# Optimization experiments

Hardware: AMD Instinct MI355X
Metric: run time of the kernel (lower is better)

The kernel has to match this reference:

```python
import jax, jax.numpy as jnp
import numpy as np

D_MODEL = 2048
N_HEADS = 32
N_KV_HEADS = 8
D_K = D_MODEL // N_HEADS
HEADS_PER_GROUP = N_HEADS // N_KV_HEADS
B, S = 2, 2048


def setup_inputs() -> dict:
    key = jax.random.key(0)
    ks = jax.random.split(key, 12)
    scale = 1.0 / np.sqrt(D_MODEL)
    inp = {
        "q": jax.random.normal(ks[0], (B, S, D_MODEL), jnp.float32),
        "k": jax.random.normal(ks[1], (B, S, D_MODEL), jnp.float32),
        "v": jax.random.normal(ks[2], (B, S, D_MODEL), jnp.float32),
        # causal mask, broadcastable over [B, H, S, S]
        "mask": jnp.tril(jnp.ones((S, S), jnp.bool_))[None, None],
        # torch Linear convention: W [out, in], y = x @ W.T + b
        "Wq": jax.random.normal(ks[3], (D_MODEL, D_MODEL), jnp.float32) * scale,
        "bq": jax.random.normal(ks[4], (D_MODEL,), jnp.float32) * 0.01,
        "Wk": jax.random.normal(ks[5], (N_KV_HEADS * D_K, D_MODEL), jnp.float32) * scale,
        "bk": jax.random.normal(ks[6], (N_KV_HEADS * D_K,), jnp.float32) * 0.01,
        "Wv": jax.random.normal(ks[7], (N_KV_HEADS * D_K, D_MODEL), jnp.float32) * scale,
        "bv": jax.random.normal(ks[8], (N_KV_HEADS * D_K,), jnp.float32) * 0.01,
        "Wo": jax.random.normal(ks[9], (D_MODEL, D_MODEL), jnp.float32) * scale,
        "bo": jax.random.normal(ks[10], (D_MODEL,), jnp.float32) * 0.01,
    }
    return inp


def reference(q, k, v, mask, Wq, bq, Wk, bk, Wv, bv, Wo, bo):
    b, s, _ = q.shape
    # projections (torch Linear: x @ W.T + b)
    query = q @ Wq.T + bq                      # [B, S, D]
    key = k @ Wk.T + bk                        # [B, S, Kv*dk]
    value = v @ Wv.T + bv
    # [B, Kv, G, S, dk] for query (group heads per kv head instead of repeating K/V)
    query = query.reshape(b, s, N_KV_HEADS, HEADS_PER_GROUP, D_K).transpose(0, 2, 3, 1, 4)
    key = key.reshape(b, s, N_KV_HEADS, D_K).transpose(0, 2, 1, 3)      # [B, Kv, S, dk]
    value = value.reshape(b, s, N_KV_HEADS, D_K).transpose(0, 2, 1, 3)  # [B, Kv, S, dk]
    scores = jnp.einsum('bkgqd,bksd->bkgqs', query, key) / jnp.sqrt(jnp.float32(D_K))
    # mask is [1,1,S,S] broadcastable; add group axis
    scores = jnp.where(mask[:, :, None], scores, jnp.float32(-1e9))
    attn = jax.nn.softmax(scores, axis=-1)     # dropout p=0.0 -> identity
    out = jnp.einsum('bkgqs,bksd->bkgqd', attn, value)  # [B, Kv, G, S, dk]
    out = out.transpose(0, 3, 1, 2, 4).reshape(b, s, D_MODEL)
    return out @ Wo.T + bo
```

## Files before the change

### kernel.cpp

```cpp
#include <hip/hip_runtime.h>
#include <cstdint>

#define D_MODEL 2048
#define NKV 8
#define GQ 4
#define DK 64
#define B_ 2
#define S_ 2048
#define MS (B_*S_)
#define KVD (NKV*DK)

typedef unsigned short u16;
typedef __attribute__((ext_vector_type(8))) short bf16x8;
typedef __attribute__((ext_vector_type(4))) short bf16x4;
typedef __attribute__((ext_vector_type(4))) float f32x4;
typedef __attribute__((ext_vector_type(16))) float f32x16;
typedef __attribute__((ext_vector_type(4))) unsigned short u16x4;

__device__ __forceinline__ u16 f2bf(float f) {
    union { float f; uint32_t u; } x; x.f = f;
    uint32_t u = x.u;
    uint32_t r = (u + 0x7FFFu + ((u >> 16) & 1u)) >> 16;
    return (u16)r;
}
__device__ __forceinline__ float bf2f(u16 h) {
    union { uint32_t u; float f; } x; x.u = ((uint32_t)h) << 16;
    return x.f;
}

__device__ __forceinline__ void gload_lds16(const void* g, void* lds) {
    __builtin_amdgcn_global_load_lds(
        (const __attribute__((address_space(1))) void*)g,
        (__attribute__((address_space(3))) void*)lds, 16, 0, 0);
}

__device__ __forceinline__ bf16x8 cvt8(float4 a, float4 b) {
    union { unsigned u[4]; bf16x8 v; } r;
    asm("v_cvt_pk_bf16_f32 %0, %1, %2" : "=v"(r.u[0]) : "v"(a.x), "v"(a.y));
    asm("v_cvt_pk_bf16_f32 %0, %1, %2" : "=v"(r.u[1]) : "v"(a.z), "v"(a.w));
    asm("v_cvt_pk_bf16_f32 %0, %1, %2" : "=v"(r.u[2]) : "v"(b.x), "v"(b.y));
    asm("v_cvt_pk_bf16_f32 %0, %1, %2" : "=v"(r.u[3]) : "v"(b.z), "v"(b.w));
    return r.v;
}

__global__ __launch_bounds__(256, 3)
void gemm_qkv(const float* __restrict__ Aq, const float* __restrict__ Ak,
              const float* __restrict__ Av,
              const float* __restrict__ Wq, const float* __restrict__ Wk,
              const float* __restrict__ Wv,
              const float* __restrict__ bq, const float* __restrict__ bk,
              const float* __restrict__ bv,
              u16* __restrict__ Qp, u16* __restrict__ Kp, u16* __restrict__ Vt) {
    __shared__ __align__(16) u16 SA[2][128 * 32];
    __shared__ __align__(16) u16 SB[2][128 * 32];
    const int tid = threadIdx.x;
    const int lane = tid & 63;
    const int fr = lane & 15, fq = lane >> 4;
    const int w = tid >> 6;
    const int wr = w >> 1, wc = w & 1;
    const int K = D_MODEL, NT = K / 32;

    const int bid = blockIdx.x;
    const int sw = (bid & 7) * 96 + (bid >> 3);
    const float* A; const float* Bw; const float* bias;
    int seg, by, bx;
    if (sw < 512)      { seg = 0; A = Aq; Bw = Wq; bias = bq; by = sw >> 4;         bx = sw & 15; }
    else if (sw < 640) { seg = 1; A = Ak; Bw = Wk; bias = bk; by = (sw - 512) >> 2; bx = (sw - 512) & 3; }
    else               { seg = 2; A = Av; Bw = Wv; bias = bv; by = (sw - 640) >> 2; bx = (sw - 640) & 3; }
    const int m0 = by * 128, n0 = bx * 128;

    const int sr = tid >> 2, sc = tid & 3;
    float4 ra[2][2], rb[2][2];
    auto LOADA = [&](int t) {
        const float* p0 = A + (size_t)(m0 + sr) * K + (t << 5) + sc * 8;
#pragma unroll
        for (int j = 0; j < 2; ++j) {
            const float* p = p0 + (size_t)(j * 64) * K;
            ra[j][0] = *(const float4*)p; ra[j][1] = *(const float4*)(p + 4);
        }
    };
    auto LOADB = [&](int t) {
        const float* p0 = Bw + (size_t)(n0 + sr) * K + (t << 5) + sc * 8;
#pragma unroll
        for (int j = 0; j < 2; ++j) {
            const float* p = p0 + (size_t)(j * 64) * K;
            rb[j][0] = *(const float4*)p; rb[j][1] = *(const float4*)(p + 4);
        }
    };
    auto WRITE = [&](int q) {
#pragma unroll
        for (int j = 0; j < 2; ++j) {
            int row = j * 64 + sr;
            int s = (sc ^ ((row >> 1) & 3)) << 4;
            *(bf16x8*)((char*)&SA[q][0] + row * 64 + s) = cvt8(ra[j][0], ra[j][1]);
            *(bf16x8*)((char*)&SB[q][0] + row * 64 + s) = cvt8(rb[j][0], rb[j][1]);
        }
    };

    f32x4 acc[4][4] = {};
    const int arow = wr * 64, brow = wc * 64;

    LOADA(0); LOADB(0);
    WRITE(0);
    LOADA(1); LOADB(1);
    asm volatile("s_waitcnt lgkmcnt(0)" ::: "memory");
    __builtin_amdgcn_s_barrier();

    for (int t = 0; t < NT; ++t) {
        const int q = t & 1;
        if (t + 1 < NT) WRITE(q ^ 1);
        if (t + 2 < NT) { LOADA(t + 2); LOADB(t + 2); }
        const char* sa = (const char*)&SA[q][0];
        const char* sb = (const char*)&SB[q][0];
        bf16x8 af[4], bfr[4];
#pragma unroll
        for (int m = 0; m < 4; ++m) {
            int row = arow + m * 16 + fr;
            af[m] = *(const bf16x8*)(sa + row * 64 + ((fq ^ ((row >> 1) & 3)) << 4));
        }
#pragma unroll
        for (int n = 0; n < 4; ++n) {
            int row = brow + n * 16 + fr;
            bfr[n] = *(const bf16x8*)(sb + row * 64 + ((fq ^ ((row >> 1) & 3)) << 4));
        }
        __builtin_amdgcn_s_setprio(1);
#pragma unroll
        for (int m = 0; m < 4; ++m)
#pragma unroll
            for (int n = 0; n < 4; ++n)
                acc[m][n] = __builtin_amdgcn_mfma_f32_16x16x32_bf16(af[m], bfr[n], acc[m][n], 0, 0, 0);
        __builtin_amdgcn_s_setprio(0);
        asm volatile("s_waitcnt lgkmcnt(0)" ::: "memory");
        __builtin_amdgcn_s_barrier();
    }

    float bvv[4];
#pragma unroll
    for (int n = 0; n < 4; ++n) bvv[n] = bias[n0 + brow + n * 16 + fr];
#pragma unroll
    for (int m = 0; m < 4; ++m) {
        int grow0 = m0 + arow + m * 16 + fq * 4;
#pragma unroll
        for (int n = 0; n < 4; ++n) {
            int gcol = n0 + brow + n * 16 + fr;
#pragma unroll
            for (int r = 0; r < 4; ++r) {
                float v = acc[m][n][r] + bvv[n];
                int grow = grow0 + r;
                if (seg == 0)      Qp[(size_t)grow * D_MODEL + gcol] = f2bf(v);
                else if (seg == 1) Kp[(size_t)grow * KVD + gcol] = f2bf(v);
                else {
                    int b = grow >> 11, s = grow & (S_ - 1);
                    Vt[((size_t)b * KVD + gcol) * S_ + s] = f2bf(v);
                }
            }
        }
    }
}

__global__ __launch_bounds__(256, 3)
void gemm_o(const u16* __restrict__ A, const float* __restrict__ Bw,
            const float* __restrict__ bias, float* __restrict__ Cout) {
    __shared__ __align__(16) u16 SA[2][128 * 32];
    __shared__ __align__(16) u16 SB[2][128 * 32];
    const int tid = threadIdx.x;
    const int lane = tid & 63;
    const int fr = lane & 15, fq = lane >> 4;
    const int w = tid >> 6;
    const int wr = w >> 1, wc = w & 1;
    const int K = D_MODEL, N = D_MODEL, NT = K / 32;

    const int bid = blockIdx.x;
    const int sw = (bid & 7) * 64 + (bid >> 3);
    const int by = sw >> 4, bx = sw & 15;
    const int m0 = by * 128, n0 = bx * 128;

    const int sr = tid >> 2, sc = tid & 3;
    bf16x8 rA[2];
    float4 rb[2][2];
    auto LOADA = [&](int t) {
        const u16* p0 = A + (size_t)(m0 + sr) * K + (t << 5) + sc * 8;
#pragma unroll
        for (int j = 0; j < 2; ++j)
            rA[j] = *(const bf16x8*)(p0 + (size_t)(j * 64) * K);
    };
    auto LOADB = [&](int t) {
        const float* p0 = Bw + (size_t)(n0 + sr) * K + (t << 5) + sc * 8;
#pragma unroll
        for (int j = 0; j < 2; ++j) {
            const float* p = p0 + (size_t)(j * 64) * K;
            rb[j][0] = *(const float4*)p; rb[j][1] = *(const float4*)(p + 4);
        }
    };
    auto WRITE = [&](int q) {
#pragma unroll
        for (int j = 0; j < 2; ++j) {
            int row = j * 64 + sr;
            int s = (sc ^ ((row >> 1) & 3)) << 4;
            *(bf16x8*)((char*)&SA[q][0] + row * 64 + s) = rA[j];
            *(bf16x8*)((char*)&SB[q][0] + row * 64 + s) = cvt8(rb[j][0], rb[j][1]);
        }
    };

    f32x4 acc[4][4] = {};
    const int arow = wr * 64, brow = wc * 64;

    LOADA(0); LOADB(0);
    WRITE(0);
    LOADA(1); LOADB(1);
    asm volatile("s_waitcnt lgkmcnt(0)" ::: "memory");
    __builtin_amdgcn_s_barrier();

    for (int t = 0; t < NT; ++t) {
        const int q = t & 1;
        if (t + 1 < NT) WRITE(q ^ 1);
        if (t + 2 < NT) { LOADA(t + 2); LOADB(t + 2); }
        const char* sa = (const char*)&SA[q][0];
        const char* sb = (const char*)&SB[q][0];
        bf16x8 af[4], bfr[4];
#pragma unroll
        for (int m = 0; m < 4; ++m) {
            int row = arow + m * 16 + fr;
            af[m] = *(const bf16x8*)(sa + row * 64 + ((fq ^ ((row >> 1) & 3)) << 4));
        }
#pragma unroll
        for (int n = 0; n < 4; ++n) {
            int row = brow + n * 16 + fr;
            bfr[n] = *(const bf16x8*)(sb + row * 64 + ((fq ^ ((row >> 1) & 3)) << 4));
        }
        __builtin_amdgcn_s_setprio(1);
#pragma unroll
        for (int m = 0; m < 4; ++m)
#pragma unroll
            for (int n = 0; n < 4; ++n)
                acc[m][n] = __builtin_amdgcn_mfma_f32_16x16x32_bf16(af[m], bfr[n], acc[m][n], 0, 0, 0);
        __builtin_amdgcn_s_setprio(0);
        asm volatile("s_waitcnt lgkmcnt(0)" ::: "memory");
        __builtin_amdgcn_s_barrier();
    }

    float bvv[4];
#pragma unroll
    for (int n = 0; n < 4; ++n) bvv[n] = bias[n0 + brow + n * 16 + fr];
#pragma unroll
    for (int m = 0; m < 4; ++m) {
        int grow0 = m0 + arow + m * 16 + fq * 4;
#pragma unroll
        for (int n = 0; n < 4; ++n) {
            int gcol = n0 + brow + n * 16 + fr;
#pragma unroll
            for (int r = 0; r < 4; ++r)
                Cout[(size_t)(grow0 + r) * N + gcol] = acc[m][n][r] + bvv[n];
        }
    }
}

__global__ __launch_bounds__(256, 4)
void attn_fwd(const u16* __restrict__ Qp, const u16* __restrict__ Kp,
              const u16* __restrict__ Vt, u16* __restrict__ AO) {
    __shared__ __align__(16) u16 Klds[2][4096];
    __shared__ __align__(16) u16 Vlds[2][4096];
    const int bid = blockIdx.x;
    const int qblk = 15 - (bid >> 6);
    const int rest = bid & 63;
    const int b = rest >> 5;
    const int kv = (rest >> 2) & 7;
    const int g = rest & 3;
    const int tid = threadIdx.x, w = tid >> 6, l = tid & 63;
    const int q31 = l & 31, hi = l >> 5;
    const int h = kv * GQ + g;
    const int qw = qblk * 128 + w * 32;
    const int q0 = qw + q31;

    const u16* kbase = Kp + (size_t)(b * S_) * KVD + kv * DK;
    const u16* vbase = Vt + ((size_t)b * KVD + kv * DK) * S_;

    const float SCALE = 0.125f * 1.44269504f;
    bf16x8 qf[4];
    const u16* qp = Qp + ((size_t)(b * S_) + q0) * D_MODEL + h * DK;
#pragma unroll
    for (int ks = 0; ks < 4; ++ks) {
        bf16x8 t = *(const bf16x8*)(qp + ks * 16 + hi * 8);
#pragma unroll
        for (int j = 0; j < 8; ++j) t[j] = (short)f2bf(bf2f((u16)t[j]) * SCALE);
        qf[ks] = t;
    }

    const int nt = 2 * qblk + 2;
    const int bound = (qw + 31) >> 6;

    auto STAGE = [&](int t, int bufsel) {
#pragma unroll
        for (int r = 0; r < 2; ++r) {
            int idx = r * 256 + tid;
            int row = idx >> 3;
            int slotK = (idx & 7) ^ (row & 7);
            int jV = (idx & 7) ^ ((row >> 1) & 7);
            u16* kdst = &Klds[bufsel][(r * 256 + w * 64) * 8];
            u16* vdst = &Vlds[bufsel][(r * 256 + w * 64) * 8];
            gload_lds16(kbase + (size_t)(t * 64 + row) * KVD + slotK * 8, kdst);
            gload_lds16(vbase + (size_t)row * S_ + t * 64 + jV * 8, vdst);
        }
    };

    f32x16 o0 = {}, o1 = {};
    float m_run = -1e30f, l_run = 0.f;

    STAGE(0, 0);
    __syncthreads();
    int cur = 0;
    for (int t = 0; t < nt; ++t) {
        if (t + 1 < nt) STAGE(t + 1, cur ^ 1);
        if (t <= bound) {
            const u16* Kc = Klds[cur];
            const u16* Vc = Vlds[cur];
            const int base0 = t * 64, base1 = t * 64 + 32;
            const bool act1 = (base1 <= qw + 31);

            f32x16 s0 = {};
            {
                const int row = q31;
#pragma unroll
                for (int ks = 0; ks < 4; ++ks) {
                    bf16x8 kf = *(const bf16x8*)&Kc[row * 64 + ((((ks << 1) | hi)) ^ (row & 7)) * 8];
                    s0 = __builtin_amdgcn_mfma_f32_32x32x16_bf16(kf, qf[ks], s0, 0, 0, 0);
                }
            }
            f32x16 s1 = {};
            if (act1) {
                const int row = 32 + q31;
#pragma unroll
                for (int ks = 0; ks < 4; ++ks) {
                    bf16x8 kf = *(const bf16x8*)&Kc[row * 64 + ((((ks << 1) | hi)) ^ (row & 7)) * 8];
                    s1 = __builtin_amdgcn_mfma_f32_32x32x16_bf16(kf, qf[ks], s1, 0, 0, 0);
                }
            }
            if (base0 + 31 > qw) {
#pragma unroll
                for (int r = 0; r < 16; ++r) {
                    int koff = (r & 3) + 8 * (r >> 2) + 4 * hi;
                    s0[r] = (base0 + koff <= q0) ? s0[r] : -1e30f;
                }
            }
            if (act1 && (base1 + 31 > qw)) {
#pragma unroll
                for (int r = 0; r < 16; ++r) {
                    int koff = (r & 3) + 8 * (r >> 2) + 4 * hi;
                    s1[r] = (base1 + koff <= q0) ? s1[r] : -1e30f;
                }
            }
            float pm = s0[0];
#pragma unroll
            for (int r = 1; r < 16; ++r) pm = fmaxf(pm, s0[r]);
            if (act1) {
#pragma unroll
                for (int r = 0; r < 16; ++r) pm = fmaxf(pm, s1[r]);
            }
            pm = fmaxf(pm, __shfl_xor(pm, 32));
            if (__any(pm > m_run + 8.0f)) {
                float mn = fmaxf(m_run, pm);
                float sc = __builtin_amdgcn_exp2f(m_run - mn);
                m_run = mn; l_run *= sc;
#pragma unroll
                for (int r = 0; r < 16; ++r) { o0[r] *= sc; o1[r] *= sc; }
            }
            float psum = 0.f;
#pragma unroll
            for (int r = 0; r < 16; ++r) { float p = __builtin_amdgcn_exp2f(s0[r] - m_run); s0[r] = p; psum += p; }
            if (act1) {
#pragma unroll
                for (int r = 0; r < 16; ++r) { float p = __builtin_amdgcn_exp2f(s1[r] - m_run); s1[r] = p; psum += p; }
            }
            l_run += psum;
            unsigned W0[8], W1[8];
#pragma unroll
            for (int tt = 0; tt < 8; ++tt)
                asm("v_cvt_pk_bf16_f32 %0, %1, %2" : "=v"(W0[tt]) : "v"(s0[2 * tt]), "v"(s0[2 * tt + 1]));
            if (act1) {
#pragma unroll
                for (int tt = 0; tt < 8; ++tt)
                    asm("v_cvt_pk_bf16_f32 %0, %1, %2" : "=v"(W1[tt]) : "v"(s1[2 * tt]), "v"(s1[2 * tt + 1]));
            }
#pragma unroll
            for (int sl = 0; sl < 2; ++sl) {
                union { unsigned u[4]; bf16x8 v; } bw;
#pragma unroll
                for (int i = 0; i < 4; ++i) bw.u[i] = W0[sl * 4 + i];
#pragma unroll
                for (int half = 0; half < 2; ++half) {
                    const int row = half * 32 + q31;
                    union { bf16x4 h4[2]; bf16x8 v; } vf;
                    int sa = (sl * 4 + hi) ^ (row & 14);
                    int sb = (sl * 4 + 2 + hi) ^ (row & 14);
                    vf.h4[0] = *(const bf16x4*)&Vc[row * 64 + sa * 4];
                    vf.h4[1] = *(const bf16x4*)&Vc[row * 64 + sb * 4];
                    if (half == 0) o0 = __builtin_amdgcn_mfma_f32_32x32x16_bf16(vf.v, bw.v, o0, 0, 0, 0);
                    else           o1 = __builtin_amdgcn_mfma_f32_32x32x16_bf16(vf.v, bw.v, o1, 0, 0, 0);
                }
            }
            if (act1) {
#pragma unroll
                for (int sl = 2; sl < 4; ++sl) {
                    union { unsigned u[4]; bf16x8 v; } bw;
#pragma unroll
                    for (int i = 0; i < 4; ++i) bw.u[i] = W1[(sl - 2) * 4 + i];
#pragma unroll
                    for (int half = 0; half < 2; ++half) {
                        const int row = half * 32 + q31;
                        union { bf16x4 h4[2]; bf16x8 v; } vf;
                        int sa = (sl * 4 + hi) ^ (row & 14);
                        int sb = (sl * 4 + 2 + hi) ^ (row & 14);
                        vf.h4[0] = *(const bf16x4*)&Vc[row * 64 + sa * 4];
                        vf.h4[1] = *(const bf16x4*)&Vc[row * 64 + sb * 4];
                        if (half == 0) o0 = __builtin_amdgcn_mfma_f32_32x32x16_bf16(vf.v, bw.v, o0, 0, 0, 0);
                        else           o1 = __builtin_amdgcn_mfma_f32_32x32x16_bf16(vf.v, bw.v, o1, 0, 0, 0);
                    }
                }
            }
        }
        __syncthreads();
        cur ^= 1;
    }

    float lt = l_run + __shfl_xor(l_run, 32);
    float rl = 1.0f / lt;
    u16* op = AO + ((size_t)(b * S_) + q0) * D_MODEL + h * DK;
#pragma unroll
    for (int half = 0; half < 2; ++half) {
#pragma unroll
        for (int rr = 0; rr < 16; rr += 4) {
            u16x4 pk;
#pragma unroll
            for (int i = 0; i < 4; ++i)
                pk[i] = f2bf((half ? o1[rr + i] : o0[rr + i]) * rl);
            *(u16x4*)(op + half * 32 + (rr >> 2) * 8 + 4 * hi) = pk;
        }
    }
}

extern "C" void kernel_launch(void* const* d_in, const int* in_sizes, int n_in,
                              void* d_out, int out_size, void* d_ws, size_t ws_size,
                              hipStream_t stream) {
    const float* q  = (const float*)d_in[0];
    const float* k  = (const float*)d_in[1];
    const float* v  = (const float*)d_in[2];
    const float* Wq = (const float*)d_in[4];
    const float* bq = (const float*)d_in[5];
    const float* Wk = (const float*)d_in[6];
    const float* bk = (const float*)d_in[7];
    const float* Wv = (const float*)d_in[8];
    const float* bv = (const float*)d_in[9];
    const float* Wo = (const float*)d_in[10];
    const float* bo = (const float*)d_in[11];
    float* out = (float*)d_out;

    char* ws = (char*)d_ws;
    size_t off = 0;
    auto alloc = [&](size_t bytes) -> void* {
        void* p = ws + off;
        off += (bytes + 255) & ~(size_t)255;
        return p;
    };
    u16* Qp = (u16*)alloc((size_t)MS * D_MODEL * 2);
    u16* Kp = (u16*)alloc((size_t)MS * KVD * 2);
    u16* Vt = (u16*)alloc((size_t)MS * KVD * 2);
    u16* AO = (u16*)alloc((size_t)MS * D_MODEL * 2);

    gemm_qkv<<<768, 256, 0, stream>>>(q, k, v, Wq, Wk, Wv, bq, bk, bv, Qp, Kp, Vt);

    attn_fwd<<<16 * 64, 256, 0, stream>>>(Qp, Kp, Vt, AO);

    gemm_o<<<512, 256, 0, stream>>>(AO, Wo, bo, out);
}
```

Measured before the change: 197.7 us.

## Stage fp32 GEMM tiles via direct global-to-LDS loads, convert to bf16 on read

Both projection GEMMs now copy fp32 tiles straight into LDS with global_load_lds and an XOR swizzle. The conversion to bf16 moves to the fragment read, replacing the previous path that loaded into registers, converted, then wrote LDS. The QKV GEMM drops its software double buffer for a single buffer with a sync before and after compute. The O GEMM keeps a two-stage pipeline controlled by vmcnt, but its larger fp32 LDS footprint lowers its launch bound from 3 to 2 blocks per SM. The aim is to cut VGPR staging and VALU conversion work, at the cost of more LDS traffic, repeated conversions per fragment, and lost load/compute overlap in the QKV kernel.

```diff
diff --git a/kernel.cpp b/kernel.cpp
--- a/kernel.cpp
+++ b/kernel.cpp
@@ -43,6 +43,14 @@
     return r.v;
 }
 
+__device__ __forceinline__ bf16x8 frag_f32(const char* S, int R, int fq) {
+    int s0 = ((2 * fq) ^ (R & 7)) * 16;
+    int s1 = ((2 * fq + 1) ^ (R & 7)) * 16;
+    float4 a = *(const float4*)(S + R * 128 + s0);
+    float4 b = *(const float4*)(S + R * 128 + s1);
+    return cvt8(a, b);
+}
+
 __global__ __launch_bounds__(256, 3)
 void gemm_qkv(const float* __restrict__ Aq, const float* __restrict__ Ak,
               const float* __restrict__ Av,
@@ -51,8 +59,8 @@
               const float* __restrict__ bq, const float* __restrict__ bk,
               const float* __restrict__ bv,
               u16* __restrict__ Qp, u16* __restrict__ Kp, u16* __restrict__ Vt) {
-    __shared__ __align__(16) u16 SA[2][128 * 32];
-    __shared__ __align__(16) u16 SB[2][128 * 32];
+    __shared__ __align__(16) char SA[128 * 128];
+    __shared__ __align__(16) char SB[128 * 128];
     const int tid = threadIdx.x;
     const int lane = tid & 63;
     const int fr = lane & 15, fq = lane >> 4;
@@ -69,60 +77,26 @@
     else               { seg = 2; A = Av; Bw = Wv; bias = bv; by = (sw - 640) >> 2; bx = (sw - 640) & 3; }
     const int m0 = by * 128, n0 = bx * 128;
 
-    const int sr = tid >> 2, sc = tid & 3;
-    float4 ra[2][2], rb[2][2];
-    auto LOADA = [&](int t) {
-        const float* p0 = A + (size_t)(m0 + sr) * K + (t << 5) + sc * 8;
-#pragma unroll
-        for (int j = 0; j < 2; ++j) {
-            const float* p = p0 + (size_t)(j * 64) * K;
-            ra[j][0] = *(const float4*)p; ra[j][1] = *(const float4*)(p + 4);
-        }
-    };
-    auto LOADB = [&](int t) {
-        const float* p0 = Bw + (size_t)(n0 + sr) * K + (t << 5) + sc * 8;
-#pragma unroll
-        for (int j = 0; j < 2; ++j) {
-            const float* p = p0 + (size_t)(j * 64) * K;
-            rb[j][0] = *(const float4*)p; rb[j][1] = *(const float4*)(p + 4);
-        }
-    };
-    auto WRITE = [&](int q) {
-#pragma unroll
-        for (int j = 0; j < 2; ++j) {
-            int row = j * 64 + sr;
-            int s = (sc ^ ((row >> 1) & 3)) << 4;
-            *(bf16x8*)((char*)&SA[q][0] + row * 64 + s) = cvt8(ra[j][0], ra[j][1]);
-            *(bf16x8*)((char*)&SB[q][0] + row * 64 + s) = cvt8(rb[j][0], rb[j][1]);
-        }
-    };
-
     f32x4 acc[4][4] = {};
     const int arow = wr * 64, brow = wc * 64;
-
-    LOADA(0); LOADB(0);
-    WRITE(0);
-    LOADA(1); LOADB(1);
-    asm volatile("s_waitcnt lgkmcnt(0)" ::: "memory");
-    __builtin_amdgcn_s_barrier();
+    const int wb16 = (tid & 192) * 16;
 
     for (int t = 0; t < NT; ++t) {
-        const int q = t & 1;
-        if (t + 1 < NT) WRITE(q ^ 1);
-        if (t + 2 < NT) { LOADA(t + 2); LOADB(t + 2); }
-        const char* sa = (const char*)&SA[q][0];
-        const char* sb = (const char*)&SB[q][0];
+        const int k0 = t << 5;
+#pragma unroll
+        for (int j = 0; j < 4; ++j) {
+            int idx = j * 256 + tid;
+            int r = idx >> 3, p = idx & 7;
+            int c = (p ^ (r & 7)) * 4;
+            gload_lds16(A  + (size_t)(m0 + r) * K + k0 + c, SA + j * 4096 + wb16);
+            gload_lds16(Bw + (size_t)(n0 + r) * K + k0 + c, SB + j * 4096 + wb16);
+        }
+        __syncthreads();
         bf16x8 af[4], bfr[4];
 #pragma unroll
-        for (int m = 0; m < 4; ++m) {
-            int row = arow + m * 16 + fr;
-            af[m] = *(const bf16x8*)(sa + row * 64 + ((fq ^ ((row >> 1) & 3)) << 4));
-        }
-#pragma unroll
-        for (int n = 0; n < 4; ++n) {
-            int row = brow + n * 16 + fr;
-            bfr[n] = *(const bf16x8*)(sb + row * 64 + ((fq ^ ((row >> 1) & 3)) << 4));
-        }
+        for (int m = 0; m < 4; ++m) af[m] = frag_f32(SA, arow + m * 16 + fr, fq);
+#pragma unroll
+        for (int n = 0; n < 4; ++n) bfr[n] = frag_f32(SB, brow + n * 16 + fr, fq);
         __builtin_amdgcn_s_setprio(1);
 #pragma unroll
         for (int m = 0; m < 4; ++m)
@@ -130,8 +104,7 @@
             for (int n = 0; n < 4; ++n)
                 acc[m][n] = __builtin_amdgcn_mfma_f32_16x16x32_bf16(af[m], bfr[n], acc[m][n], 0, 0, 0);
         __builtin_amdgcn_s_setprio(0);
-        asm volatile("s_waitcnt lgkmcnt(0)" ::: "memory");
-        __builtin_amdgcn_s_barrier();
+        __syncthreads();
     }
 
     float bvv[4];
@@ -158,11 +131,11 @@
     }
 }
 
-__global__ __launch_bounds__(256, 3)
+__global__ __launch_bounds__(256, 2)
 void gemm_o(const u16* __restrict__ A, const float* __restrict__ Bw,
             const float* __restrict__ bias, float* __restrict__ Cout) {
-    __shared__ __align__(16) u16 SA[2][128 * 32];
-    __shared__ __align__(16) u16 SB[2][128 * 32];
+    __shared__ __align__(16) char SAo[2][128 * 64];
+    __shared__ __align__(16) char SBo[2][128 * 128];
     const int tid = threadIdx.x;
     const int lane = tid & 63;
     const int fr = lane & 15, fq = lane >> 4;
@@ -174,60 +147,45 @@
     const int sw = (bid & 7) * 64 + (bid >> 3);
     const int by = sw >> 4, bx = sw & 15;
     const int m0 = by * 128, n0 = bx * 128;
-
-    const int sr = tid >> 2, sc = tid & 3;
-    bf16x8 rA[2];
-    float4 rb[2][2];
-    auto LOADA = [&](int t) {
-        const u16* p0 = A + (size_t)(m0 + sr) * K + (t << 5) + sc * 8;
-#pragma unroll
-        for (int j = 0; j < 2; ++j)
-            rA[j] = *(const bf16x8*)(p0 + (size_t)(j * 64) * K);
-    };
-    auto LOADB = [&](int t) {
-        const float* p0 = Bw + (size_t)(n0 + sr) * K + (t << 5) + sc * 8;
+    const int wb16 = (tid & 192) * 16;
+
+    auto STAGE = [&](int t, int qb) {
+        const int k0 = t << 5;
 #pragma unroll
         for (int j = 0; j < 2; ++j) {
-            const float* p = p0 + (size_t)(j * 64) * K;
-            rb[j][0] = *(const float4*)p; rb[j][1] = *(const float4*)(p + 4);
-        }
-    };
-    auto WRITE = [&](int q) {
-#pragma unroll
-        for (int j = 0; j < 2; ++j) {
-            int row = j * 64 + sr;
-            int s = (sc ^ ((row >> 1) & 3)) << 4;
-            *(bf16x8*)((char*)&SA[q][0] + row * 64 + s) = rA[j];
-            *(bf16x8*)((char*)&SB[q][0] + row * 64 + s) = cvt8(rb[j][0], rb[j][1]);
+            int idx = j * 256 + tid;
+            int r = idx >> 2, p = idx & 3;
+            gload_lds16(A + (size_t)(m0 + r) * K + k0 + p * 8, SAo[qb] + j * 4096 + wb16);
+        }
+#pragma unroll
+        for (int j = 0; j < 4; ++j) {
+            int idx = j * 256 + tid;
+            int r = idx >> 3, p = idx & 7;
+            int c = (p ^ (r & 7)) * 4;
+            gload_lds16(Bw + (size_t)(n0 + r) * K + k0 + c, SBo[qb] + j * 4096 + wb16);
         }
     };
 
     f32x4 acc[4][4] = {};
     const int arow = wr * 64, brow = wc * 64;
 
-    LOADA(0); LOADB(0);
-    WRITE(0);
-    LOADA(1); LOADB(1);
-    asm volatile("s_waitcnt lgkmcnt(0)" ::: "memory");
+    STAGE(0, 0);
+    STAGE(1, 1);
+    asm volatile("s_waitcnt vmcnt(6)" ::: "memory");
     __builtin_amdgcn_s_barrier();
 
     for (int t = 0; t < NT; ++t) {
-        const int q = t & 1;
-        if (t + 1 < NT) WRITE(q ^ 1);
-        if (t + 2 < NT) { LOADA(t + 2); LOADB(t + 2); }
-        const char* sa = (const char*)&SA[q][0];
-        const char* sb = (const char*)&SB[q][0];
+        const int qb = t & 1;
+        const char* sa = SAo[qb];
+        const char* sb = SBo[qb];
         bf16x8 af[4], bfr[4];
 #pragma unroll
         for (int m = 0; m < 4; ++m) {
-            int row = arow + m * 16 + fr;
-            af[m] = *(const bf16x8*)(sa + row * 64 + ((fq ^ ((row >> 1) & 3)) << 4));
-        }
-#pragma unroll
-        for (int n = 0; n < 4; ++n) {
-            int row = brow + n * 16 + fr;
-            bfr[n] = *(const bf16x8*)(sb + row * 64 + ((fq ^ ((row >> 1) & 3)) << 4));
-        }
+            int R = arow + m * 16 + fr;
+            af[m] = *(const bf16x8*)(sa + R * 64 + fq * 16);
+        }
+#pragma unroll
+        for (int n = 0; n < 4; ++n) bfr[n] = frag_f32(sb, brow + n * 16 + fr, fq);
         __builtin_amdgcn_s_setprio(1);
 #pragma unroll
         for (int m = 0; m < 4; ++m)
@@ -235,8 +193,16 @@
             for (int n = 0; n < 4; ++n)
                 acc[m][n] = __builtin_amdgcn_mfma_f32_16x16x32_bf16(af[m], bfr[n], acc[m][n], 0, 0, 0);
         __builtin_amdgcn_s_setprio(0);
-        asm volatile("s_waitcnt lgkmcnt(0)" ::: "memory");
-        __builtin_amdgcn_s_barrier();
+        if (t + 1 < NT) {
+            __builtin_amdgcn_s_barrier();
+            if (t + 2 < NT) {
+                STAGE(t + 2, qb);
+                asm volatile("s_waitcnt vmcnt(6)" ::: "memory");
+            } else {
+                asm volatile("s_waitcnt vmcnt(0)" ::: "memory");
+            }
+            __builtin_amdgcn_s_barrier();
+        }
     }
 
     float bvv[4];
```

Result: slower. 219.1 us (+10.8%).
